# Kernel optimization log

Hardware: AMD Instinct MI355X
Metric: run time of the kernel (lower is better)

## Reference

```python
import jax, jax.numpy as jnp
import numpy as np

EPS = 1e-5

def _ln(x, g, b):
    m = jnp.mean(x, axis=-1, keepdims=True)
    v = jnp.var(x, axis=-1, keepdims=True)
    return (x - m) / jnp.sqrt(v + EPS) * g + b

def setup_inputs() -> dict:
    key = jax.random.key(0)
    ks = jax.random.split(key, 16)
    B, T, N, K, d, E = 2, 12, 512, 8, 64, 64
    D = K * d
    s = 0.02
    inp = {
        "x": jax.random.normal(ks[0], (B, T, N, D), jnp.float32),
        "lapmatrix": jax.random.normal(ks[1], (N, N), jnp.float32),
        "node_embeddings": jax.random.normal(ks[2], (N, E), jnp.float32),
        "Wq": jax.random.normal(ks[3], (D, D), jnp.float32) * s,
        "bq": jnp.zeros((D,), jnp.float32),
        "Wk": jax.random.normal(ks[4], (D, D), jnp.float32) * s,
        "bk": jnp.zeros((D,), jnp.float32),
        "Wv": jax.random.normal(ks[5], (D, D), jnp.float32) * s,
        "bv": jnp.zeros((D,), jnp.float32),
        "Wo": jax.random.normal(ks[6], (D, D), jnp.float32) * s,
        "bo": jnp.zeros((D,), jnp.float32),
        "W1": jax.random.normal(ks[7], (4 * D, D), jnp.float32) * s,
        "b1": jnp.zeros((4 * D,), jnp.float32),
        "W2": jax.random.normal(ks[8], (D, 4 * D), jnp.float32) * s,
        "b2": jnp.zeros((D,), jnp.float32),
        "g1": jnp.ones((D,), jnp.float32),
        "be1": jnp.zeros((D,), jnp.float32),
        "g2": jnp.ones((D,), jnp.float32),
        "be2": jnp.zeros((D,), jnp.float32),
        "alpha": jnp.float32(1.0),
        "beta": jnp.float32(1.0),
        "k": 3,
    }
    return inp

def reference(x, lapmatrix, node_embeddings, Wq, bq, Wk, bk, Wv, bv, Wo, bo,
              W1, b1, W2, b2, g1, be1, g2, be2, alpha, beta, k):
    B, T, N, D = x.shape
    K, d = 8, D // 8
    x_raw = x
    xn = _ln(x, g1, be1)
    q = (xn @ Wq.T + bq).reshape(B, T, N, K, d)
    kk = (xn @ Wk.T + bk).reshape(B, T, N, K, d)
    v = (xn @ Wv.T + bv).reshape(B, T, N, K, d)
    # raw attention logits: [B,T,K,N,N]
    raw = jnp.einsum('btnkd,btmkd->btknm', q, kk) / jnp.sqrt(jnp.float32(d))
    # graph biases, all [N,N], broadcast over B,T,K
    supports = jax.nn.softmax(jax.nn.relu(node_embeddings @ node_embeddings.T), axis=1)
    adj = (lapmatrix != 0).astype(x.dtype)
    mask = jnp.where(adj == 0, jnp.float32(-1e9), jnp.float32(0.0))
    logits = raw + alpha * supports + beta * lapmatrix + mask
    attn = jax.nn.softmax(logits, axis=-1)  # dropout = identity in eval
    out = jnp.einsum('btknm,btmkd->btnkd', attn, v).reshape(B, T, N, D)
    x1 = x_raw + (out @ Wo.T + bo)
    h = _ln(x1, g2, be2)
    ffn = jax.nn.relu(h @ W1.T + b1) @ W2.T + b2
    return x1 + ffn
```

## Files before the change

### kernel.cpp

```cpp
#include <hip/hip_runtime.h>

typedef unsigned short u16;
typedef unsigned int   u32;
typedef __attribute__((ext_vector_type(8))) short bf16x8;
typedef __attribute__((ext_vector_type(4))) float f32x4;

#define DEV static __device__ __forceinline__

DEV float b2f(u16 u){ return __uint_as_float(((u32)u)<<16); }
DEV u16 f2b(float f){
  u32 u = __float_as_uint(f);
  u32 r = (u + 0x7FFFu + ((u>>16)&1u)) >> 16;
  return (u16)r;
}

union V8 { uint4 v; u16 s[8]; };

DEV u32 cvt_pk_bf16(float lo, float hi){
  u32 r;
  asm("v_cvt_pk_bf16_f32 %0, %1, %2" : "=v"(r) : "v"(lo), "v"(hi));
  return r;
}

DEV bool is_f32(const void* dt){ return *(const u32*)dt == 0x3F800000u; }

DEV uint4 ld8_ext_bf(const void* p, size_t i, bool f32){
  if(f32){
    const float* q = (const float*)p + i;
    float4 a = *(const float4*)q, b = *(const float4*)(q+4);
    V8 r;
    r.s[0]=f2b(a.x); r.s[1]=f2b(a.y); r.s[2]=f2b(a.z); r.s[3]=f2b(a.w);
    r.s[4]=f2b(b.x); r.s[5]=f2b(b.y); r.s[6]=f2b(b.z); r.s[7]=f2b(b.w);
    return r.v;
  }
  return *(const uint4*)((const u16*)p + i);
}
DEV void ld8_ext_f(const void* p, size_t i, bool f32, float* o){
  if(f32){
    const float* q = (const float*)p + i;
    float4 a = *(const float4*)q, b = *(const float4*)(q+4);
    o[0]=a.x;o[1]=a.y;o[2]=a.z;o[3]=a.w;o[4]=b.x;o[5]=b.y;o[6]=b.z;o[7]=b.w;
  }else{
    V8 u; u.v = *(const uint4*)((const u16*)p + i);
    #pragma unroll
    for(int k=0;k<8;k++) o[k]=b2f(u.s[k]);
  }
}
DEV float ld1_ext(const void* p, size_t i, bool f32){
  return f32 ? ((const float*)p)[i] : b2f(((const u16*)p)[i]);
}
DEV float load_scalar(const void* p, bool f32){
  return f32 ? *(const float*)p : b2f(*(const u16*)p);
}

DEV void gl_lds16(const u16* g, u16* l){
  __builtin_amdgcn_global_load_lds((const __attribute__((address_space(1))) void*)g,
                                   (__attribute__((address_space(3))) void*)l, 16, 0, 0);
}

__global__ __launch_bounds__(256) void sentinel_kernel(u16* out, long n, const void* dt){
  long ne = is_f32(dt) ? 2*n : n;
  long i = (long)blockIdx.x*256 + threadIdx.x;
  if(i < ne) out[i] = 0x4442;
}

__global__ __launch_bounds__(256) void convert_w_kernel(
    const void* Wq, const void* Wk, const void* Wv, const void* Wo,
    const void* W1, const void* W2, u16* __restrict__ wbf, const void* dt)
{
  const bool f32 = is_f32(dt);
  size_t i = ((size_t)blockIdx.x*256 + threadIdx.x)*8;
  const void* src; size_t base;
  if(i < 262144){ src=Wq; base=0; }
  else if(i < 524288){ src=Wk; base=262144; }
  else if(i < 786432){ src=Wv; base=524288; }
  else if(i < 1048576){ src=Wo; base=786432; }
  else if(i < 2097152){ src=W1; base=1048576; }
  else { src=W2; base=2097152; }
  *(uint4*)(wbf + i) = ld8_ext_bf(src, i-base, f32);
}

__global__ __launch_bounds__(256) void convert_b_kernel(
    const void* bq, const void* bk, const void* bv, const void* bo,
    const void* b1, const void* b2, float* __restrict__ bfp, const void* dt)
{
  const bool f32 = is_f32(dt);
  int j = blockIdx.x*256 + threadIdx.x;
  if(j >= 4608) return;
  const void* src; int off;
  if(j < 512){ src=bq; off=0; }
  else if(j < 1024){ src=bk; off=512; }
  else if(j < 1536){ src=bv; off=1024; }
  else if(j < 2048){ src=bo; off=1536; }
  else if(j < 4096){ src=b1; off=2048; }
  else { src=b2; off=4096; }
  bfp[j] = ld1_ext(src, j-off, f32);
}

__global__ __launch_bounds__(256) void bias_kernel(
    const void* __restrict__ E, const void* __restrict__ lap,
    const void* __restrict__ alpha_p, const void* __restrict__ beta_p,
    float* __restrict__ bm, const void* dt)
{
  __shared__ u16 Et[64*520];
  __shared__ float red[8];
  const bool f32 = is_f32(dt);
  const int t = threadIdx.x, n = blockIdx.x;
  for(int i=0;i<16;i++){
    int c = t + i*256;
    int m = c >> 3, j0 = (c & 7) * 8;
    V8 u; u.v = ld8_ext_bf(E, (size_t)m*64 + j0, f32);
    #pragma unroll
    for(int jj=0;jj<8;jj++) Et[(j0+jj)*520 + m] = u.s[jj];
  }
  __syncthreads();
  const float alpha = load_scalar(alpha_p, f32);
  const float beta  = load_scalar(beta_p, f32);
  float sc0=0.f, sc1=0.f;
  const int m0 = t, m1 = t+256;
  for(int kk=0;kk<64;kk++){
    float en = b2f(Et[kk*520+n]);
    sc0 += en * b2f(Et[kk*520+m0]);
    sc1 += en * b2f(Et[kk*520+m1]);
  }
  sc0 = fmaxf(sc0, 0.f); sc1 = fmaxf(sc1, 0.f);
  float mx = fmaxf(sc0, sc1);
  for(int o=1;o<64;o<<=1) mx = fmaxf(mx, __shfl_xor(mx,o,64));
  const int wave = t>>6;
  if((t&63)==0) red[wave]=mx;
  __syncthreads();
  mx = fmaxf(fmaxf(red[0],red[1]), fmaxf(red[2],red[3]));
  float e0 = __expf(sc0-mx), e1 = __expf(sc1-mx);
  float sm = e0+e1;
  for(int o=1;o<64;o<<=1) sm += __shfl_xor(sm,o,64);
  if((t&63)==0) red[4+wave]=sm;
  __syncthreads();
  sm = red[4]+red[5]+red[6]+red[7];
  const float inv = 1.f/sm;
  const int q0b = n>>5, iq = (n>>4)&1, l16 = n&15;
  const size_t qpart = (size_t)q0b*256 + (size_t)l16*4 + iq;
  float lv0 = ld1_ext(lap, (size_t)n*512+m0, f32);
  {
    float val = alpha*e0*inv + beta*lv0 + (lv0==0.f ? -1e9f : 0.f);
    int kb = m0>>3, e = m0&7;
    bm[(size_t)kb*4096 + qpart + (e>>1)*64 + (e&1)*2] = val;
  }
  float lv1 = ld1_ext(lap, (size_t)n*512+m1, f32);
  {
    float val = alpha*e1*inv + beta*lv1 + (lv1==0.f ? -1e9f : 0.f);
    int kb = m1>>3, e = m1&7;
    bm[(size_t)kb*4096 + qpart + (e>>1)*64 + (e&1)*2] = val;
  }
}

template<int EXTIN>
__global__ __launch_bounds__(64) void ln_kernel(const void* __restrict__ xin,
    const void* __restrict__ g, const void* __restrict__ b, u16* __restrict__ out,
    const void* dt)
{
  const bool f32 = is_f32(dt);
  const int row = blockIdx.x, lane = threadIdx.x;
  float v[8];
  if(EXTIN){
    ld8_ext_f(xin, (size_t)row*512 + lane*8, f32, v);
  }else{
    V8 u; u.v = *(const uint4*)((const u16*)xin + (size_t)row*512 + lane*8);
    #pragma unroll
    for(int i=0;i<8;i++) v[i]=b2f(u.s[i]);
  }
  float s=0.f, ss=0.f;
  #pragma unroll
  for(int i=0;i<8;i++){ s+=v[i]; ss+=v[i]*v[i]; }
  #pragma unroll
  for(int o=1;o<64;o<<=1){ s+=__shfl_xor(s,o,64); ss+=__shfl_xor(ss,o,64); }
  const float mean = s*(1.0f/512.0f);
  const float var  = ss*(1.0f/512.0f) - mean*mean;
  const float rstd = rsqrtf(var + 1e-5f);
  float gv[8], bv[8];
  ld8_ext_f(g, (size_t)lane*8, f32, gv);
  ld8_ext_f(b, (size_t)lane*8, f32, bv);
  V8 o8;
  #pragma unroll
  for(int i=0;i<8;i++) o8.s[i]=f2b((v[i]-mean)*rstd*gv[i]+bv[i]);
  *(uint4*)(out+(size_t)row*512+lane*8)=o8.v;
}

template<int RELU, int RES, int RESEXT, int OUTEXT>
__global__ __launch_bounds__(256) void gemm_nt(
    const u16* __restrict__ A, const u16* __restrict__ B,
    const float* __restrict__ bias, const void* __restrict__ resid,
    void* __restrict__ Cout, int N, int K, const void* dt)
{
  __shared__ u16 As[128*64];
  __shared__ u16 Bs[128*64];
  const bool f32 = is_f32(dt);
  const int t = threadIdx.x;
  const int wave = t>>6, lane = t&63;
  const int n0 = blockIdx.y*128, m0 = blockIdx.x*128;
  const int wr = wave>>1, wc = wave&1;

  f32x4 acc[4][4];
  #pragma unroll
  for(int i=0;i<4;i++)
    #pragma unroll
    for(int j=0;j<4;j++){ acc[i][j][0]=0.f; acc[i][j][1]=0.f; acc[i][j][2]=0.f; acc[i][j][3]=0.f; }

  const int lrow8 = lane>>3, lg = lane&7;
  const int gsw = (lg ^ lrow8)*8;
  const u16* Ag = A + (size_t)(m0+lrow8)*K + gsw;
  const u16* Bg = B + (size_t)(n0+lrow8)*K + gsw;
  const int fr = lane&15, qd = lane>>4, frk = (fr&7);

  for(int k0=0; k0<K; k0+=64){
    __syncthreads();
    #pragma unroll
    for(int i=0;i<4;i++){
      int c = wave*4+i;
      gl_lds16(Ag + (size_t)(c*8)*K + k0, &As[c*512]);
      gl_lds16(Bg + (size_t)(c*8)*K + k0, &Bs[c*512]);
    }
    __syncthreads();
    #pragma unroll
    for(int s=0;s<2;s++){
      const int slot = ((s*4+qd) ^ frk)*8;
      bf16x8 af[4], bfr[4];
      #pragma unroll
      for(int i=0;i<4;i++) af[i] = *(const bf16x8*)&As[(wr*64+i*16+fr)*64 + slot];
      #pragma unroll
      for(int j=0;j<4;j++) bfr[j] = *(const bf16x8*)&Bs[(wc*64+j*16+fr)*64 + slot];
      #pragma unroll
      for(int i=0;i<4;i++)
        #pragma unroll
        for(int j=0;j<4;j++)
          acc[i][j] = __builtin_amdgcn_mfma_f32_16x16x32_bf16(af[i], bfr[j], acc[i][j], 0,0,0);
    }
  }

  const int col16 = lane&15, rbase = (lane>>4)*4;
  #pragma unroll
  for(int i=0;i<4;i++){
    #pragma unroll
    for(int j=0;j<4;j++){
      const int gc = n0 + wc*64 + j*16 + col16;
      const float bv = bias[gc];
      #pragma unroll
      for(int r=0;r<4;r++){
        const int gr = m0 + wr*64 + i*16 + rbase + r;
        float val = acc[i][j][r] + bv;
        if(RELU) val = fmaxf(val, 0.f);
        if(RES){
          if(RESEXT) val += ld1_ext(resid, (size_t)gr*N+gc, f32);
          else       val += b2f(((const u16*)resid)[(size_t)gr*N+gc]);
        }
        if(OUTEXT && f32) ((float*)Cout)[(size_t)gr*N+gc] = val;
        else              ((u16*)Cout)[(size_t)gr*N+gc] = f2b(val);
      }
    }
  }
}

template<int RELU, int RES, int RESEXT, int OUTEXT>
__global__ __launch_bounds__(256) void gemm_nt64(
    const u16* __restrict__ A, const u16* __restrict__ B,
    const float* __restrict__ bias, const void* __restrict__ resid,
    void* __restrict__ Cout, int N, int K, const void* dt)
{
  __shared__ u16 As[128*64];
  __shared__ u16 Bs[64*64];
  const bool f32 = is_f32(dt);
  const int t = threadIdx.x;
  const int wave = t>>6, lane = t&63;
  const int n0 = blockIdx.y*64, m0 = blockIdx.x*128;
  const int wr = wave>>1, wc = wave&1;

  f32x4 acc[4][2];
  #pragma unroll
  for(int i=0;i<4;i++)
    #pragma unroll
    for(int j=0;j<2;j++){ acc[i][j][0]=0.f; acc[i][j][1]=0.f; acc[i][j][2]=0.f; acc[i][j][3]=0.f; }

  const int lrow8 = lane>>3, lg = lane&7;
  const int gsw = (lg ^ lrow8)*8;
  const u16* Ag = A + (size_t)(m0+lrow8)*K + gsw;
  const u16* Bg = B + (size_t)(n0+lrow8)*K + gsw;
  const int fr = lane&15, qd = lane>>4, frk = (fr&7);

  for(int k0=0; k0<K; k0+=64){
    __syncthreads();
    #pragma unroll
    for(int i=0;i<4;i++){
      int c = wave*4+i;
      gl_lds16(Ag + (size_t)(c*8)*K + k0, &As[c*512]);
    }
    #pragma unroll
    for(int i=0;i<2;i++){
      int c = wave*2+i;
      gl_lds16(Bg + (size_t)(c*8)*K + k0, &Bs[c*512]);
    }
    __syncthreads();
    #pragma unroll
    for(int s=0;s<2;s++){
      const int slot = ((s*4+qd) ^ frk)*8;
      bf16x8 af[4], bfr[2];
      #pragma unroll
      for(int i=0;i<4;i++) af[i] = *(const bf16x8*)&As[(wr*64+i*16+fr)*64 + slot];
      #pragma unroll
      for(int j=0;j<2;j++) bfr[j] = *(const bf16x8*)&Bs[(wc*32+j*16+fr)*64 + slot];
      #pragma unroll
      for(int i=0;i<4;i++)
        #pragma unroll
        for(int j=0;j<2;j++)
          acc[i][j] = __builtin_amdgcn_mfma_f32_16x16x32_bf16(af[i], bfr[j], acc[i][j], 0,0,0);
    }
  }

  const int col16 = lane&15, rbase = (lane>>4)*4;
  #pragma unroll
  for(int i=0;i<4;i++){
    #pragma unroll
    for(int j=0;j<2;j++){
      const int gc = n0 + wc*32 + j*16 + col16;
      const float bv = bias[gc];
      #pragma unroll
      for(int r=0;r<4;r++){
        const int gr = m0 + wr*64 + i*16 + rbase + r;
        float val = acc[i][j][r] + bv;
        if(RELU) val = fmaxf(val, 0.f);
        if(RES){
          if(RESEXT) val += ld1_ext(resid, (size_t)gr*N+gc, f32);
          else       val += b2f(((const u16*)resid)[(size_t)gr*N+gc]);
        }
        if(OUTEXT && f32) ((float*)Cout)[(size_t)gr*N+gc] = val;
        else              ((u16*)Cout)[(size_t)gr*N+gc] = f2b(val);
      }
    }
  }
}

__global__ __launch_bounds__(256,3) void attn_kernel(
    const u16* __restrict__ qkv, const float* __restrict__ bm,
    u16* __restrict__ out)
{
  __shared__ u16 Kb[128*64];
  __shared__ u16 Vt[2][64*136];

  const int QS = 1536;
  const int t = threadIdx.x, wave = t>>6, lane = t&63;
  const int head = blockIdx.x, bt = blockIdx.z;
  const int q0 = blockIdx.y*128 + wave*32;
  const u16* qp = qkv + (size_t)bt*512*QS + head*64;
  const u16* kp = qp + 512;
  const u16* vp = qp + 1024;

  const int l16 = lane&15, qd = lane>>4;

  const int lrow8 = lane>>3, lg = lane&7;
  const int srow = t & 127;
  const int shalf = (t >> 7) * 32;
  const u16* vcp = vp + (size_t)srow*QS + shalf;

  #pragma unroll
  for(int ii=0;ii<4;ii++){
    const int c8 = wave*4 + ii;
    const int pg = lg ^ ((2*(lrow8&3) + (c8&3)) & 7);
    gl_lds16(kp + (size_t)(c8*8 + lrow8)*QS + pg*8, &Kb[c8*512]);
  }
  uint4 vv[4];
  #pragma unroll
  for(int qi=0;qi<4;qi++) vv[qi] = *(const uint4*)(vcp + qi*8);

  bf16x8 qf[2][2];
  #pragma unroll
  for(int i=0;i<2;i++)
    #pragma unroll
    for(int kc=0;kc<2;kc++)
      qf[i][kc] = *(const bf16x8*)(qp + (size_t)(q0 + i*16 + l16)*QS + kc*32 + qd*8);

  const float* bml = bm + (size_t)(blockIdx.y*4 + wave)*256 + (size_t)qd*4096 + (size_t)l16*4;

  const int arow = ((l16>>2)<<3) + (l16&3);
  const int rperm = (2*(l16&3) + (l16>>2)) & 7;
  const int g0 = (qd ^ rperm)*8;
  const u16* KA0 = &Kb[arow*64 + g0];
  const u16* KA1 = &Kb[arow*64 + (g0 ^ 32)];

  float mrun[2], lrun[2];
  mrun[0] = -3e38f; mrun[1] = -3e38f;
  lrun[0] = 0.f;    lrun[1] = 0.f;
  f32x4 oacc[2][4];
  #pragma unroll
  for(int i=0;i<2;i++)
    #pragma unroll
    for(int j=0;j<4;j++){ oacc[i][j][0]=0.f; oacc[i][j][1]=0.f; oacc[i][j][2]=0.f; oacc[i][j][3]=0.f; }

  #pragma unroll
  for(int qi=0;qi<4;qi++){
    V8 u; u.v = vv[qi];
    #pragma unroll
    for(int jj=0;jj<8;jj++) Vt[0][(shalf + qi*8 + jj)*136 + srow] = u.s[jj];
  }
  __syncthreads();

  #pragma unroll
  for(int c=0;c<4;c++){
    f32x4 p[2][8];
    __builtin_amdgcn_s_setprio(1);
    #pragma unroll
    for(int tt=0;tt<8;tt++){
      const int ro = (tt&3)*2048 + (tt>>2)*256;
      bf16x8 a0 = *(const bf16x8*)(KA0 + ro);
      bf16x8 a1 = *(const bf16x8*)(KA1 + ro);
      #pragma unroll
      for(int i=0;i<2;i++){
        f32x4 s; s[0]=0.f; s[1]=0.f; s[2]=0.f; s[3]=0.f;
        s = __builtin_amdgcn_mfma_f32_16x16x32_bf16(a0, qf[i][0], s, 0,0,0);
        s = __builtin_amdgcn_mfma_f32_16x16x32_bf16(a1, qf[i][1], s, 0,0,0);
        p[i][tt] = s;
      }
    }
    __builtin_amdgcn_s_setprio(0);
    if(c<3){
      __syncthreads();
      #pragma unroll
      for(int ii=0;ii<4;ii++){
        const int c8 = wave*4 + ii;
        const int pg = lg ^ ((2*(lrow8&3) + (c8&3)) & 7);
        gl_lds16(kp + (size_t)((c+1)*128 + c8*8 + lrow8)*QS + pg*8, &Kb[c8*512]);
      }
      #pragma unroll
      for(int qi=0;qi<4;qi++) vv[qi] = *(const uint4*)(vcp + (size_t)((c+1)*128)*QS + qi*8);
    }

    float mx0 = -3e38f, mx1 = -3e38f;
    #pragma unroll
    for(int s4=0;s4<4;s4++){
      const float* bp = bml + c*65536 + s4*16384;
      const float4 bg0 = *(const float4*)(bp);
      const float4 bg1 = *(const float4*)(bp + 64);
      const float4 bg2 = *(const float4*)(bp + 128);
      const float4 bg3 = *(const float4*)(bp + 192);
      #pragma unroll
      for(int i=0;i<2;i++){
        f32x4& pl = p[i][s4];
        pl[0] = pl[0]*0.125f + (i ? bg0.y : bg0.x);
        pl[1] = pl[1]*0.125f + (i ? bg0.w : bg0.z);
        pl[2] = pl[2]*0.125f + (i ? bg1.y : bg1.x);
        pl[3] = pl[3]*0.125f + (i ? bg1.w : bg1.z);
        f32x4& ph = p[i][s4+4];
        ph[0] = ph[0]*0.125f + (i ? bg2.y : bg2.x);
        ph[1] = ph[1]*0.125f + (i ? bg2.w : bg2.z);
        ph[2] = ph[2]*0.125f + (i ? bg3.y : bg3.x);
        ph[3] = ph[3]*0.125f + (i ? bg3.w : bg3.z);
        const float m8 = fmaxf(fmaxf(fmaxf(pl[0],pl[1]),fmaxf(pl[2],pl[3])),
                               fmaxf(fmaxf(ph[0],ph[1]),fmaxf(ph[2],ph[3])));
        if(i==0) mx0 = fmaxf(mx0, m8); else mx1 = fmaxf(mx1, m8);
      }
    }

    #pragma unroll
    for(int i=0;i<2;i++){
      float mx = i ? mx1 : mx0;
      mx = fmaxf(mx, __shfl_xor(mx, 16, 64));
      mx = fmaxf(mx, __shfl_xor(mx, 32, 64));
      const float mnew = fmaxf(mrun[i], mx);
      if(__any(mx > mrun[i])){
        const float al = __expf(mrun[i] - mnew);
        lrun[i] *= al;
        #pragma unroll
        for(int r=0;r<4;r++){
          const float alr = __shfl(al, (qd<<2)+r, 64);
          #pragma unroll
          for(int j=0;j<4;j++) oacc[i][j][r] *= alr;
        }
      }
      mrun[i] = mnew;
      float rs = 0.f;
      #pragma unroll
      for(int tt=0;tt<8;tt++){
        p[i][tt][0] = __expf(p[i][tt][0]-mnew);
        p[i][tt][1] = __expf(p[i][tt][1]-mnew);
        p[i][tt][2] = __expf(p[i][tt][2]-mnew);
        p[i][tt][3] = __expf(p[i][tt][3]-mnew);
        rs += (p[i][tt][0]+p[i][tt][1]) + (p[i][tt][2]+p[i][tt][3]);
      }
      rs += __shfl_xor(rs, 16, 64);
      rs += __shfl_xor(rs, 32, 64);
      lrun[i] += rs;
    }

    __builtin_amdgcn_s_setprio(1);
    #pragma unroll
    for(int ks=0;ks<4;ks++){
      union { bf16x8 v; u32 w[4]; } pa[2];
      #pragma unroll
      for(int i=0;i<2;i++){
        pa[i].w[0] = cvt_pk_bf16(p[i][ks][0],   p[i][ks][1]);
        pa[i].w[1] = cvt_pk_bf16(p[i][ks][2],   p[i][ks][3]);
        pa[i].w[2] = cvt_pk_bf16(p[i][ks+4][0], p[i][ks+4][1]);
        pa[i].w[3] = cvt_pk_bf16(p[i][ks+4][2], p[i][ks+4][3]);
      }
      #pragma unroll
      for(int j=0;j<4;j++){
        bf16x8 bvf = *(const bf16x8*)&Vt[c&1][(j*16 + l16)*136 + ks*32 + qd*8];
        oacc[0][j] = __builtin_amdgcn_mfma_f32_16x16x32_bf16(pa[0].v, bvf, oacc[0][j], 0,0,0);
        oacc[1][j] = __builtin_amdgcn_mfma_f32_16x16x32_bf16(pa[1].v, bvf, oacc[1][j], 0,0,0);
      }
    }
    __builtin_amdgcn_s_setprio(0);

    if(c<3){
      #pragma unroll
      for(int qi=0;qi<4;qi++){
        V8 u; u.v = vv[qi];
        #pragma unroll
        for(int jj=0;jj<8;jj++) Vt[(c+1)&1][(shalf + qi*8 + jj)*136 + srow] = u.s[jj];
      }
      __syncthreads();
    }
  }

  u16* op = out + (size_t)bt*512*512 + head*64;
  #pragma unroll
  for(int i=0;i<2;i++){
    const float inv = 1.f / lrun[i];
    #pragma unroll
    for(int r=0;r<4;r++){
      const float invr = __shfl(inv, (qd<<2)+r, 64);
      const size_t rowb = (size_t)(q0 + i*16 + qd*4 + r)*512;
      #pragma unroll
      for(int j=0;j<4;j++)
        op[rowb + j*16 + l16] = f2b(oacc[i][j][r] * invr);
    }
  }
}

extern "C" void kernel_launch(void* const* d_in, const int* in_sizes, int n_in,
                              void* d_out, int out_size, void* d_ws, size_t ws_size,
                              hipStream_t stream) {
  const void* x   = d_in[0];
  const void* lap = d_in[1];
  const void* ne  = d_in[2];
  const void* Wq  = d_in[3];
  const void* bq  = d_in[4];
  const void* Wk  = d_in[5];
  const void* bk  = d_in[6];
  const void* Wv  = d_in[7];
  const void* bv  = d_in[8];
  const void* Wo  = d_in[9];
  const void* bo  = d_in[10];
  const void* W1  = d_in[11];
  const void* b1  = d_in[12];
  const void* W2  = d_in[13];
  const void* b2  = d_in[14];
  const void* g1  = d_in[15];
  const void* be1 = d_in[16];
  const void* g2  = d_in[17];
  const void* be2 = d_in[18];
  const void* alpha = d_in[19];
  const void* beta  = d_in[20];
  const void* dt = g1;

  const int M = 12288;
  const size_t NEED = (size_t)512*512*4 + (size_t)M*512*2*2 + (size_t)M*2048*2
                    + (size_t)3145728*2 + (size_t)4608*4;
  if(ws_size < NEED){
    long n = out_size;
    sentinel_kernel<<<(2*n+255)/256, 256, 0, stream>>>((u16*)d_out, n, dt);
    return;
  }
  char* w = (char*)d_ws;
  float* bias_m = (float*)w;              w += (size_t)512*512*4;
  u16*   slotB  = (u16*)w;                w += (size_t)M*512*2;
  char*  slotC  = w;                      w += (size_t)M*2048*2;
  u16*   x1     = (u16*)w;                w += (size_t)M*512*2;
  u16*   wbf    = (u16*)w;                w += (size_t)3145728*2;
  float* bfp    = (float*)w;
  u16* qkv = (u16*)slotC;
  u16* h1  = (u16*)slotC;
  u16* xn = slotB;
  u16* ao = slotB;
  u16* h  = slotB;

  convert_w_kernel<<<1536, 256, 0, stream>>>(Wq, Wk, Wv, Wo, W1, W2, wbf, dt);
  convert_b_kernel<<<18, 256, 0, stream>>>(bq, bk, bv, bo, b1, b2, bfp, dt);
  bias_kernel<<<512, 256, 0, stream>>>(ne, lap, alpha, beta, bias_m, dt);
  ln_kernel<1><<<M, 64, 0, stream>>>(x, g1, be1, xn, dt);
  gemm_nt<0,0,0,0><<<dim3(96,12), 256, 0, stream>>>(xn, wbf, bfp, nullptr, qkv, 1536, 512, dt);
  attn_kernel<<<dim3(8,4,24), 256, 0, stream>>>(qkv, bias_m, ao);
  gemm_nt64<0,1,1,0><<<dim3(96,8), 256, 0, stream>>>(ao, wbf+786432, bfp+1536, x, x1, 512, 512, dt);
  ln_kernel<0><<<M, 64, 0, stream>>>(x1, g2, be2, h, dt);
  gemm_nt<1,0,0,0><<<dim3(96,16), 256, 0, stream>>>(h, wbf+1048576, bfp+2048, nullptr, h1, 2048, 512, dt);
  gemm_nt64<0,1,0,1><<<dim3(96,8), 256, 0, stream>>>(h1, wbf+2097152, bfp+4096, x1, d_out, 512, 2048, dt);
}
```

Baseline: 329.6 us.

## Merge weight/bias conversion, graph bias, and first LayerNorm into one prep kernel

Four independent preprocessing kernels (weight conversion, bias conversion, graph-bias softmax, first LayerNorm) are combined into a single launch that dispatches on block index. This removes three kernel launches and lets the independent tasks run concurrently on the GPU. The LayerNorm now handles four rows per 256-thread block instead of one row per 64-thread block, and the node-embedding bias path reads E directly from global memory instead of transposing it into shared memory. The single-pass variance (E[x^2]-mean^2) may differ slightly numerically from a two-pass form.

```diff
diff --git a/kernel.cpp b/kernel.cpp
--- a/kernel.cpp
+++ b/kernel.cpp
@@ -64,92 +64,105 @@
   if(i < ne) out[i] = 0x4442;
 }
 
-__global__ __launch_bounds__(256) void convert_w_kernel(
+__global__ __launch_bounds__(256) void prep_kernel(
+    const void* __restrict__ x, const void* __restrict__ g1,
+    const void* __restrict__ be1, u16* __restrict__ xn,
     const void* Wq, const void* Wk, const void* Wv, const void* Wo,
-    const void* W1, const void* W2, u16* __restrict__ wbf, const void* dt)
-{
-  const bool f32 = is_f32(dt);
-  size_t i = ((size_t)blockIdx.x*256 + threadIdx.x)*8;
-  const void* src; size_t base;
-  if(i < 262144){ src=Wq; base=0; }
-  else if(i < 524288){ src=Wk; base=262144; }
-  else if(i < 786432){ src=Wv; base=524288; }
-  else if(i < 1048576){ src=Wo; base=786432; }
-  else if(i < 2097152){ src=W1; base=1048576; }
-  else { src=W2; base=2097152; }
-  *(uint4*)(wbf + i) = ld8_ext_bf(src, i-base, f32);
-}
-
-__global__ __launch_bounds__(256) void convert_b_kernel(
+    const void* W1, const void* W2, u16* __restrict__ wbf,
     const void* bq, const void* bk, const void* bv, const void* bo,
-    const void* b1, const void* b2, float* __restrict__ bfp, const void* dt)
-{
-  const bool f32 = is_f32(dt);
-  int j = blockIdx.x*256 + threadIdx.x;
-  if(j >= 4608) return;
-  const void* src; int off;
-  if(j < 512){ src=bq; off=0; }
-  else if(j < 1024){ src=bk; off=512; }
-  else if(j < 1536){ src=bv; off=1024; }
-  else if(j < 2048){ src=bo; off=1536; }
-  else if(j < 4096){ src=b1; off=2048; }
-  else { src=b2; off=4096; }
-  bfp[j] = ld1_ext(src, j-off, f32);
-}
-
-__global__ __launch_bounds__(256) void bias_kernel(
+    const void* b1, const void* b2, float* __restrict__ bfp,
     const void* __restrict__ E, const void* __restrict__ lap,
     const void* __restrict__ alpha_p, const void* __restrict__ beta_p,
     float* __restrict__ bm, const void* dt)
 {
-  __shared__ u16 Et[64*520];
+  __shared__ float En[64];
   __shared__ float red[8];
   const bool f32 = is_f32(dt);
-  const int t = threadIdx.x, n = blockIdx.x;
-  for(int i=0;i<16;i++){
-    int c = t + i*256;
-    int m = c >> 3, j0 = (c & 7) * 8;
-    V8 u; u.v = ld8_ext_bf(E, (size_t)m*64 + j0, f32);
-    #pragma unroll
-    for(int jj=0;jj<8;jj++) Et[(j0+jj)*520 + m] = u.s[jj];
-  }
-  __syncthreads();
-  const float alpha = load_scalar(alpha_p, f32);
-  const float beta  = load_scalar(beta_p, f32);
-  float sc0=0.f, sc1=0.f;
-  const int m0 = t, m1 = t+256;
-  for(int kk=0;kk<64;kk++){
-    float en = b2f(Et[kk*520+n]);
-    sc0 += en * b2f(Et[kk*520+m0]);
-    sc1 += en * b2f(Et[kk*520+m1]);
-  }
-  sc0 = fmaxf(sc0, 0.f); sc1 = fmaxf(sc1, 0.f);
-  float mx = fmaxf(sc0, sc1);
-  for(int o=1;o<64;o<<=1) mx = fmaxf(mx, __shfl_xor(mx,o,64));
-  const int wave = t>>6;
-  if((t&63)==0) red[wave]=mx;
-  __syncthreads();
-  mx = fmaxf(fmaxf(red[0],red[1]), fmaxf(red[2],red[3]));
-  float e0 = __expf(sc0-mx), e1 = __expf(sc1-mx);
-  float sm = e0+e1;
-  for(int o=1;o<64;o<<=1) sm += __shfl_xor(sm,o,64);
-  if((t&63)==0) red[4+wave]=sm;
-  __syncthreads();
-  sm = red[4]+red[5]+red[6]+red[7];
-  const float inv = 1.f/sm;
-  const int q0b = n>>5, iq = (n>>4)&1, l16 = n&15;
-  const size_t qpart = (size_t)q0b*256 + (size_t)l16*4 + iq;
-  float lv0 = ld1_ext(lap, (size_t)n*512+m0, f32);
-  {
-    float val = alpha*e0*inv + beta*lv0 + (lv0==0.f ? -1e9f : 0.f);
-    int kb = m0>>3, e = m0&7;
-    bm[(size_t)kb*4096 + qpart + (e>>1)*64 + (e&1)*2] = val;
-  }
-  float lv1 = ld1_ext(lap, (size_t)n*512+m1, f32);
-  {
-    float val = alpha*e1*inv + beta*lv1 + (lv1==0.f ? -1e9f : 0.f);
-    int kb = m1>>3, e = m1&7;
-    bm[(size_t)kb*4096 + qpart + (e>>1)*64 + (e&1)*2] = val;
+  const int bid = blockIdx.x, t = threadIdx.x;
+
+  if(bid < 3072){
+    const int row = bid*4 + (t>>6), lane = t&63;
+    float v[8];
+    ld8_ext_f(x, (size_t)row*512 + lane*8, f32, v);
+    float s=0.f, ss=0.f;
+    #pragma unroll
+    for(int i=0;i<8;i++){ s+=v[i]; ss+=v[i]*v[i]; }
+    #pragma unroll
+    for(int o=1;o<64;o<<=1){ s+=__shfl_xor(s,o,64); ss+=__shfl_xor(ss,o,64); }
+    const float mean = s*(1.0f/512.0f);
+    const float var  = ss*(1.0f/512.0f) - mean*mean;
+    const float rstd = rsqrtf(var + 1e-5f);
+    float gv[8], bv[8];
+    ld8_ext_f(g1, (size_t)lane*8, f32, gv);
+    ld8_ext_f(be1, (size_t)lane*8, f32, bv);
+    V8 o8;
+    #pragma unroll
+    for(int i=0;i<8;i++) o8.s[i]=f2b((v[i]-mean)*rstd*gv[i]+bv[i]);
+    *(uint4*)(xn+(size_t)row*512+lane*8)=o8.v;
+  } else if(bid < 4608){
+    size_t i = ((size_t)(bid-3072)*256 + t)*8;
+    const void* src; size_t base;
+    if(i < 262144){ src=Wq; base=0; }
+    else if(i < 524288){ src=Wk; base=262144; }
+    else if(i < 786432){ src=Wv; base=524288; }
+    else if(i < 1048576){ src=Wo; base=786432; }
+    else if(i < 2097152){ src=W1; base=1048576; }
+    else { src=W2; base=2097152; }
+    *(uint4*)(wbf + i) = ld8_ext_bf(src, i-base, f32);
+  } else if(bid < 5120){
+    const int n = bid - 4608;
+    if(t < 64) En[t] = ld1_ext(E, (size_t)n*64 + t, f32);
+    __syncthreads();
+    const float alpha = load_scalar(alpha_p, f32);
+    const float beta  = load_scalar(beta_p, f32);
+    const int m0 = t, m1 = t+256;
+    float sc0=0.f, sc1=0.f;
+    #pragma unroll
+    for(int c=0;c<8;c++){
+      float a0[8], a1[8];
+      ld8_ext_f(E, (size_t)m0*64 + c*8, f32, a0);
+      ld8_ext_f(E, (size_t)m1*64 + c*8, f32, a1);
+      #pragma unroll
+      for(int j=0;j<8;j++){ const float en = En[c*8+j]; sc0 += en*a0[j]; sc1 += en*a1[j]; }
+    }
+    sc0 = fmaxf(sc0, 0.f); sc1 = fmaxf(sc1, 0.f);
+    float mx = fmaxf(sc0, sc1);
+    for(int o=1;o<64;o<<=1) mx = fmaxf(mx, __shfl_xor(mx,o,64));
+    const int wave = t>>6;
+    if((t&63)==0) red[wave]=mx;
+    __syncthreads();
+    mx = fmaxf(fmaxf(red[0],red[1]), fmaxf(red[2],red[3]));
+    float e0 = __expf(sc0-mx), e1 = __expf(sc1-mx);
+    float sm = e0+e1;
+    for(int o=1;o<64;o<<=1) sm += __shfl_xor(sm,o,64);
+    if((t&63)==0) red[4+wave]=sm;
+    __syncthreads();
+    sm = red[4]+red[5]+red[6]+red[7];
+    const float inv = 1.f/sm;
+    const int q0b = n>>5, iq = (n>>4)&1, l16 = n&15;
+    const size_t qpart = (size_t)q0b*256 + (size_t)l16*4 + iq;
+    float lv0 = ld1_ext(lap, (size_t)n*512+m0, f32);
+    {
+      float val = alpha*e0*inv + beta*lv0 + (lv0==0.f ? -1e9f : 0.f);
+      int kb = m0>>3, e = m0&7;
+      bm[(size_t)kb*4096 + qpart + (e>>1)*64 + (e&1)*2] = val;
+    }
+    float lv1 = ld1_ext(lap, (size_t)n*512+m1, f32);
+    {
+      float val = alpha*e1*inv + beta*lv1 + (lv1==0.f ? -1e9f : 0.f);
+      int kb = m1>>3, e = m1&7;
+      bm[(size_t)kb*4096 + qpart + (e>>1)*64 + (e&1)*2] = val;
+    }
+  } else {
+    int j = (bid-5120)*256 + t;
+    const void* src; int off;
+    if(j < 512){ src=bq; off=0; }
+    else if(j < 1024){ src=bk; off=512; }
+    else if(j < 1536){ src=bv; off=1024; }
+    else if(j < 2048){ src=bo; off=1536; }
+    else if(j < 4096){ src=b1; off=2048; }
+    else { src=b2; off=4096; }
+    bfp[j] = ld1_ext(src, j-off, f32);
   }
 }
 
@@ -581,10 +594,11 @@
   u16* ao = slotB;
   u16* h  = slotB;
 
-  convert_w_kernel<<<1536, 256, 0, stream>>>(Wq, Wk, Wv, Wo, W1, W2, wbf, dt);
-  convert_b_kernel<<<18, 256, 0, stream>>>(bq, bk, bv, bo, b1, b2, bfp, dt);
-  bias_kernel<<<512, 256, 0, stream>>>(ne, lap, alpha, beta, bias_m, dt);
-  ln_kernel<1><<<M, 64, 0, stream>>>(x, g1, be1, xn, dt);
+  prep_kernel<<<5138, 256, 0, stream>>>(
+      x, g1, be1, xn,
+      Wq, Wk, Wv, Wo, W1, W2, wbf,
+      bq, bk, bv, bo, b1, b2, bfp,
+      ne, lap, alpha, beta, bias_m, dt);
   gemm_nt<0,0,0,0><<<dim3(96,12), 256, 0, stream>>>(xn, wbf, bfp, nullptr, qkv, 1536, 512, dt);
   attn_kernel<<<dim3(8,4,24), 256, 0, stream>>>(qkv, bias_m, ao);
   gemm_nt64<0,1,1,0><<<dim3(96,8), 256, 0, stream>>>(ao, wbf+786432, bfp+1536, x, x1, 512, 512, dt);
```

After: 328.3 us. No clear change (-0.4%).
